# Kernel optimization log

Measured on AMD Instinct MI355X. Metric: run time of the kernel, lower is better.

The kernel has to match this reference:

```python
import jax, jax.numpy as jnp
import numpy as np

N_CODES = 1024
CODE_DIM = 256
B, T = 64, 1024


def setup_inputs() -> dict:
    key = jax.random.key(0)
    k1, k2 = jax.random.split(key)
    inputs = jax.random.normal(k1, (B, CODE_DIM, T), dtype=jnp.float32)
    embed = jax.random.normal(k2, (N_CODES, CODE_DIM), dtype=jnp.float32)
    return {"inputs": inputs, "embed": embed, "training": 0}


def reference(inputs, embed, training):
    # inputs: [B, D, T] -> [B, T, D]
    x = jnp.transpose(inputs, (0, 2, 1))
    Bsz, Tlen, D = x.shape
    flat = x.reshape(-1, D)  # [N, D], N = B*T
    distances = (
        jnp.sum(flat * flat, axis=1, keepdims=True)
        - 2.0 * jnp.matmul(flat, embed.T)
        + jnp.sum(embed * embed, axis=1)
    )  # [N, n_codes]
    encoding_indices = jnp.argmin(distances, axis=1)  # [N]
    # gather instead of one-hot matmul (same math)
    quantized = embed[encoding_indices].reshape(x.shape)  # [B, T, D]

    sg = jax.lax.stop_gradient
    codebook_loss = jnp.mean((sg(quantized) - x) ** 2)
    cmt_loss = jnp.mean((quantized - sg(x)) ** 2)
    loss = codebook_loss + cmt_loss * 0.2

    # straight-through estimator
    quantized_st = x + sg(quantized - x)
    quantized_out = jnp.transpose(quantized_st, (0, 2, 1))  # [B, D, T]

    # avg one-hot probabilities via bincount-style scatter-add
    n = flat.shape[0]
    counts = jnp.zeros((N_CODES,), dtype=flat.dtype).at[encoding_indices].add(1.0)
    avg_probs = counts / n
    perplexity = jnp.exp(-jnp.sum(avg_probs * jnp.log(avg_probs + 1e-10)))

    encoding_indices_out = encoding_indices.reshape(Bsz, -1, 1)
    return (quantized_out, loss, cmt_loss, encoding_indices_out, perplexity)
```

## Files before the change

kernel.cpp:

```cpp
#include <hip/hip_runtime.h>

#define B_ 64
#define D_ 256
#define T_ 1024
#define NC_ 1024
#define DT_ (D_ * T_)
#define NPTS_ (B_ * T_)

#define QSZ_   16777216
#define LOSS_OFF 16777216
#define CMT_OFF  16777217
#define IDX_OFF  16777218
#define PERP_OFF 16842754

typedef _Float16 half8 __attribute__((ext_vector_type(8)));
typedef float f32x4 __attribute__((ext_vector_type(4)));

__global__ void prep_embed(const float* __restrict__ embed,
                           _Float16* __restrict__ ehi,
                           _Float16* __restrict__ elo,
                           float* __restrict__ normf) {
  int g = blockIdx.x;
  int tid = threadIdx.x;
  int w = tid >> 6, l = tid & 63;

#pragma unroll
  for (int ii = 0; ii < 2; ++ii) {
    int kc = w * 2 + ii;
    int code = g * 16 + (l & 15);
    int k0 = kc * 32 + (l >> 4) * 8;
    const float* src = embed + (size_t)code * D_ + k0;
    half8 hh, ll;
#pragma unroll
    for (int j = 0; j < 8; ++j) {
      float v = src[j];
      _Float16 h = (_Float16)v;
      _Float16 lo = (_Float16)(v - (float)h);
      hh[j] = h;
      ll[j] = lo;
    }
    size_t off = ((size_t)(g * 8 + kc) * 64 + l) * 8;
    *(half8*)(ehi + off) = hh;
    *(half8*)(elo + off) = ll;
  }

  int code = g * 16 + (tid >> 4);
  int ks = (tid & 15) * 16;
  const float* src = embed + (size_t)code * D_ + ks;
  double s = 0.0;
#pragma unroll
  for (int j = 0; j < 16; ++j) {
    double v = src[j];
    s += v * v;
  }
#pragma unroll
  for (int m = 1; m < 16; m <<= 1) s += __shfl_xor(s, m, 64);
  if ((tid & 15) == 0) normf[code] = (float)s;
}

__device__ __forceinline__ void gld_lds16(const _Float16* gsrc_lane,
                                          _Float16* lds_base) {
  __builtin_amdgcn_global_load_lds(
      (const __attribute__((address_space(1))) void*)gsrc_lane,
      (__attribute__((address_space(3))) void*)lds_base, 16, 0, 0);
}

__global__ __launch_bounds__(256, 3) void argmin_kernel(
    const float* __restrict__ inputs, const _Float16* __restrict__ ehi,
    const _Float16* __restrict__ elo, const float* __restrict__ normf,
    float* __restrict__ idx_out, int* __restrict__ counts,
    double* __restrict__ mse_acc) {
  __shared__ _Float16 ldsB[2][8192];
  __shared__ float normf_lds[1024];
  __shared__ double xn2w[64];

  int tid = threadIdx.x;
  int blk = blockIdx.x;
  int b = blk >> 4, t0 = (blk & 15) * 64;
  int w = tid >> 6, l = tid & 63;

  half8 ah[8], al[8];
  double xn2p = 0.0;
  {
    const float* xsrc = inputs + (size_t)b * DT_ + t0 + w * 16 + (l & 15);
    int kbase = (l >> 4) * 8;
#pragma unroll
    for (int kc = 0; kc < 8; ++kc) {
      half8 hh, ll;
#pragma unroll
      for (int j = 0; j < 8; ++j) {
        float v = xsrc[(size_t)(kc * 32 + kbase + j) * T_];
        xn2p += (double)v * v;
        _Float16 h = (_Float16)v;
        _Float16 lo = (_Float16)(v - (float)h);
        hh[j] = h;
        ll[j] = lo;
      }
      ah[kc] = hh;
      al[kc] = ll;
    }
  }
  xn2p += __shfl_xor(xn2p, 16, 64);
  xn2p += __shfl_xor(xn2p, 32, 64);
  if (l < 16) xn2w[w * 16 + l] = xn2p;

  ((float4*)normf_lds)[tid] = ((const float4*)normf)[tid];
#pragma unroll
  for (int i = 0; i < 2; ++i) {
    int kc = w * 2 + i;
    size_t off = ((size_t)kc * 64 + l) * 8;
    gld_lds16(ehi + off, &ldsB[0][kc * 512]);
    gld_lds16(elo + off, &ldsB[0][4096 + kc * 512]);
  }
  __syncthreads();

  float bestv[4];
  int besti[4];
#pragma unroll
  for (int j = 0; j < 4; ++j) {
    bestv[j] = 1e30f;
    besti[j] = 0;
  }

#pragma unroll 1
  for (int t = 0; t < 64; ++t) {
    int cur = t & 1, nxt = cur ^ 1;
    if (t < 63) {
#pragma unroll
      for (int i = 0; i < 2; ++i) {
        int kc = w * 2 + i;
        size_t off = ((size_t)((t + 1) * 8 + kc) * 64 + l) * 8;
        gld_lds16(ehi + off, &ldsB[nxt][kc * 512]);
        gld_lds16(elo + off, &ldsB[nxt][4096 + kc * 512]);
      }
    }

    f32x4 acc = (f32x4){0.f, 0.f, 0.f, 0.f};
#pragma unroll
    for (int kc = 0; kc < 8; ++kc) {
      half8 bh = *(const half8*)&ldsB[cur][(kc * 64 + l) * 8];
      half8 bl = *(const half8*)&ldsB[cur][4096 + (kc * 64 + l) * 8];
      acc = __builtin_amdgcn_mfma_f32_16x16x32_f16(ah[kc], bh, acc, 0, 0, 0);
      acc = __builtin_amdgcn_mfma_f32_16x16x32_f16(al[kc], bh, acc, 0, 0, 0);
      acc = __builtin_amdgcn_mfma_f32_16x16x32_f16(ah[kc], bl, acc, 0, 0, 0);
    }

    {
      int c = t * 16 + (l & 15);
      float nf = normf_lds[c];
#pragma unroll
      for (int j = 0; j < 4; ++j) {
        float df = fmaf(-2.0f, acc[j], nf);
        if (df < bestv[j]) {
          bestv[j] = df;
          besti[j] = c;
        }
      }
    }
    __syncthreads();
  }

#pragma unroll
  for (int msk = 1; msk < 16; msk <<= 1) {
#pragma unroll
    for (int j = 0; j < 4; ++j) {
      float ov = __shfl_xor(bestv[j], msk, 64);
      int oi = __shfl_xor(besti[j], msk, 64);
      if (ov < bestv[j] || (ov == bestv[j] && oi < besti[j])) {
        bestv[j] = ov;
        besti[j] = oi;
      }
    }
  }

  if ((l & 15) == 0) {
    float4 iw;
    double s = 0.0;
#pragma unroll
    for (int j = 0; j < 4; ++j) {
      int p = (l >> 4) * 4 + j;
      iw[j == 0 ? 0 : (j == 1 ? 1 : (j == 2 ? 2 : 3))] = (float)besti[j];
      atomicAdd(&counts[besti[j]], 1);
      s += xn2w[w * 16 + p] + (double)bestv[j];
    }
    *(float4*)&idx_out[blk * 64 + w * 16 + (l >> 4) * 4] = iw;
    s += __shfl_xor(s, 16, 64);
    s += __shfl_xor(s, 32, 64);
    if (l == 0) atomicAdd(mse_acc, s);
  }
}

__global__ __launch_bounds__(256) void quantize_kernel(
    const float* __restrict__ embed, const float* __restrict__ idx_f,
    float* __restrict__ qout) {
  __shared__ float qs[64 * 257];
  __shared__ int lidx[64];

  int tid = threadIdx.x;
  int bx = blockIdx.x;
  int b = bx >> 4;
  int t0 = (bx & 15) * 64;

  if (tid < 64) lidx[tid] = (int)idx_f[b * T_ + t0 + tid];
  __syncthreads();

#pragma unroll 4
  for (int p = 0; p < 64; ++p) {
    qs[p * 257 + tid] = embed[(size_t)lidx[p] * D_ + tid];
  }
  __syncthreads();

  size_t base = (size_t)b * DT_ + t0;
#pragma unroll 4
  for (int i = 0; i < 64; ++i) {
    int d = i * 4 + (tid >> 6);
    int p = tid & 63;
    qout[base + (size_t)d * T_ + p] = qs[p * 257 + d];
  }
}

__global__ void finalize_kernel(const int* __restrict__ counts,
                                const double* __restrict__ mse_acc,
                                float* __restrict__ out) {
  int tid = threadIdx.x;
  double p = (double)counts[tid] / (double)NPTS_;
  double s = p * log(p + 1e-10);
  for (int m = 32; m; m >>= 1) s += __shfl_down(s, m, 64);
  __shared__ double red[16];
  if ((tid & 63) == 0) red[tid >> 6] = s;
  __syncthreads();
  if (tid == 0) {
    double tot = 0.0;
    for (int i = 0; i < 16; ++i) tot += red[i];
    double mse = *mse_acc / (double)QSZ_;
    out[LOSS_OFF] = (float)(mse * 1.2);
    out[CMT_OFF] = (float)mse;
    out[PERP_OFF] = (float)exp(-tot);
  }
}

extern "C" void kernel_launch(void* const* d_in, const int* in_sizes, int n_in,
                              void* d_out, int out_size, void* d_ws,
                              size_t ws_size, hipStream_t stream) {
  const float* inputs = (const float*)d_in[0];
  const float* embed = (const float*)d_in[1];
  float* out = (float*)d_out;

  char* ws = (char*)d_ws;
  _Float16* ehi = (_Float16*)ws;
  _Float16* elo = (_Float16*)(ws + 524288);
  float* normf = (float*)(ws + 1048576);
  int* counts = (int*)(ws + 1048576 + 4096);
  double* mse = (double*)(ws + 1048576 + 8192);

  hipMemsetAsync(ws + 1048576 + 4096, 0, 4096 + 8, stream);

  prep_embed<<<64, 256, 0, stream>>>(embed, ehi, elo, normf);
  argmin_kernel<<<1024, 256, 0, stream>>>(inputs, ehi, elo, normf,
                                          out + IDX_OFF, counts, mse);
  quantize_kernel<<<1024, 256, 0, stream>>>(embed, out + IDX_OFF, out);
  finalize_kernel<<<1, 1024, 0, stream>>>(counts, mse, out);
}
```

Before: 176.8 us.

## Process two 16-row M tiles per wave in argmin to reuse codebook fragments

Each wave now holds A fragments for 32 points instead of 16 and runs two accumulator chains over every codebook tile loaded into LDS. The number of blocks is halved. This amortizes LDS reads of the codebook and the per-block codebook streaming over twice as many points, and interleaves independent MFMAs to hide their latency. In exchange it doubles A-fragment registers and lowers the occupancy target from 3 to 2 blocks per CU. With 512 blocks the grid may also underfill the GPU.

```diff
diff --git a/kernel.cpp b/kernel.cpp
--- a/kernel.cpp
+++ b/kernel.cpp
@@ -65,44 +65,52 @@
       (__attribute__((address_space(3))) void*)lds_base, 16, 0, 0);
 }
 
-__global__ __launch_bounds__(256, 3) void argmin_kernel(
+__global__ __launch_bounds__(256, 2) void argmin_kernel(
     const float* __restrict__ inputs, const _Float16* __restrict__ ehi,
     const _Float16* __restrict__ elo, const float* __restrict__ normf,
     float* __restrict__ idx_out, int* __restrict__ counts,
     double* __restrict__ mse_acc) {
   __shared__ _Float16 ldsB[2][8192];
   __shared__ float normf_lds[1024];
-  __shared__ double xn2w[64];
+  __shared__ double xn2w[128];
 
   int tid = threadIdx.x;
   int blk = blockIdx.x;
-  int b = blk >> 4, t0 = (blk & 15) * 64;
+  int b = blk >> 3, t0 = (blk & 7) * 128;
   int w = tid >> 6, l = tid & 63;
 
-  half8 ah[8], al[8];
-  double xn2p = 0.0;
+  half8 ah[2][8], al[2][8];
+  double xn2p0 = 0.0, xn2p1 = 0.0;
   {
-    const float* xsrc = inputs + (size_t)b * DT_ + t0 + w * 16 + (l & 15);
-    int kbase = (l >> 4) * 8;
-#pragma unroll
-    for (int kc = 0; kc < 8; ++kc) {
-      half8 hh, ll;
-#pragma unroll
-      for (int j = 0; j < 8; ++j) {
-        float v = xsrc[(size_t)(kc * 32 + kbase + j) * T_];
-        xn2p += (double)v * v;
-        _Float16 h = (_Float16)v;
-        _Float16 lo = (_Float16)(v - (float)h);
-        hh[j] = h;
-        ll[j] = lo;
-      }
-      ah[kc] = hh;
-      al[kc] = ll;
-    }
-  }
-  xn2p += __shfl_xor(xn2p, 16, 64);
-  xn2p += __shfl_xor(xn2p, 32, 64);
-  if (l < 16) xn2w[w * 16 + l] = xn2p;
+    int kq = (l >> 4) * 8;
+    const float* xcol = inputs + (size_t)b * DT_ + t0 + w * 32 + (l & 15);
+#pragma unroll
+    for (int m = 0; m < 2; ++m) {
+      const float* src = xcol + m * 16;
+#pragma unroll
+      for (int kc = 0; kc < 8; ++kc) {
+        half8 hh, ll;
+#pragma unroll
+        for (int j = 0; j < 8; ++j) {
+          float v = src[(size_t)(kc * 32 + kq + j) * T_];
+          if (m == 0) xn2p0 += (double)v * v; else xn2p1 += (double)v * v;
+          _Float16 h = (_Float16)v;
+          hh[j] = h;
+          ll[j] = (_Float16)(v - (float)h);
+        }
+        ah[m][kc] = hh;
+        al[m][kc] = ll;
+      }
+    }
+  }
+  xn2p0 += __shfl_xor(xn2p0, 16, 64);
+  xn2p0 += __shfl_xor(xn2p0, 32, 64);
+  xn2p1 += __shfl_xor(xn2p1, 16, 64);
+  xn2p1 += __shfl_xor(xn2p1, 32, 64);
+  if (l < 16) {
+    xn2w[w * 32 + l] = xn2p0;
+    xn2w[w * 32 + 16 + l] = xn2p1;
+  }
 
   ((float4*)normf_lds)[tid] = ((const float4*)normf)[tid];
 #pragma unroll
@@ -114,13 +122,15 @@
   }
   __syncthreads();
 
-  float bestv[4];
-  int besti[4];
-#pragma unroll
-  for (int j = 0; j < 4; ++j) {
-    bestv[j] = 1e30f;
-    besti[j] = 0;
-  }
+  float bestv[2][4];
+  int besti[2][4];
+#pragma unroll
+  for (int m = 0; m < 2; ++m)
+#pragma unroll
+    for (int j = 0; j < 4; ++j) {
+      bestv[m][j] = 1e30f;
+      besti[m][j] = 0;
+    }
 
 #pragma unroll 1
   for (int t = 0; t < 64; ++t) {
@@ -135,14 +145,18 @@
       }
     }
 
-    f32x4 acc = (f32x4){0.f, 0.f, 0.f, 0.f};
+    f32x4 acc0 = (f32x4){0.f, 0.f, 0.f, 0.f};
+    f32x4 acc1 = (f32x4){0.f, 0.f, 0.f, 0.f};
 #pragma unroll
     for (int kc = 0; kc < 8; ++kc) {
       half8 bh = *(const half8*)&ldsB[cur][(kc * 64 + l) * 8];
       half8 bl = *(const half8*)&ldsB[cur][4096 + (kc * 64 + l) * 8];
-      acc = __builtin_amdgcn_mfma_f32_16x16x32_f16(ah[kc], bh, acc, 0, 0, 0);
-      acc = __builtin_amdgcn_mfma_f32_16x16x32_f16(al[kc], bh, acc, 0, 0, 0);
-      acc = __builtin_amdgcn_mfma_f32_16x16x32_f16(ah[kc], bl, acc, 0, 0, 0);
+      acc0 = __builtin_amdgcn_mfma_f32_16x16x32_f16(ah[0][kc], bh, acc0, 0, 0, 0);
+      acc1 = __builtin_amdgcn_mfma_f32_16x16x32_f16(ah[1][kc], bh, acc1, 0, 0, 0);
+      acc0 = __builtin_amdgcn_mfma_f32_16x16x32_f16(al[0][kc], bh, acc0, 0, 0, 0);
+      acc1 = __builtin_amdgcn_mfma_f32_16x16x32_f16(al[1][kc], bh, acc1, 0, 0, 0);
+      acc0 = __builtin_amdgcn_mfma_f32_16x16x32_f16(ah[0][kc], bl, acc0, 0, 0, 0);
+      acc1 = __builtin_amdgcn_mfma_f32_16x16x32_f16(ah[1][kc], bl, acc1, 0, 0, 0);
     }
 
     {
@@ -150,10 +164,15 @@
       float nf = normf_lds[c];
 #pragma unroll
       for (int j = 0; j < 4; ++j) {
-        float df = fmaf(-2.0f, acc[j], nf);
-        if (df < bestv[j]) {
-          bestv[j] = df;
-          besti[j] = c;
+        float df0 = fmaf(-2.0f, acc0[j], nf);
+        if (df0 < bestv[0][j]) {
+          bestv[0][j] = df0;
+          besti[0][j] = c;
+        }
+        float df1 = fmaf(-2.0f, acc1[j], nf);
+        if (df1 < bestv[1][j]) {
+          bestv[1][j] = df1;
+          besti[1][j] = c;
         }
       }
     }
@@ -163,27 +182,33 @@
 #pragma unroll
   for (int msk = 1; msk < 16; msk <<= 1) {
 #pragma unroll
-    for (int j = 0; j < 4; ++j) {
-      float ov = __shfl_xor(bestv[j], msk, 64);
-      int oi = __shfl_xor(besti[j], msk, 64);
-      if (ov < bestv[j] || (ov == bestv[j] && oi < besti[j])) {
-        bestv[j] = ov;
-        besti[j] = oi;
-      }
-    }
+    for (int m = 0; m < 2; ++m)
+#pragma unroll
+      for (int j = 0; j < 4; ++j) {
+        float ov = __shfl_xor(bestv[m][j], msk, 64);
+        int oi = __shfl_xor(besti[m][j], msk, 64);
+        if (ov < bestv[m][j] || (ov == bestv[m][j] && oi < besti[m][j])) {
+          bestv[m][j] = ov;
+          besti[m][j] = oi;
+        }
+      }
   }
 
   if ((l & 15) == 0) {
-    float4 iw;
+    int q = l >> 4;
     double s = 0.0;
 #pragma unroll
-    for (int j = 0; j < 4; ++j) {
-      int p = (l >> 4) * 4 + j;
-      iw[j == 0 ? 0 : (j == 1 ? 1 : (j == 2 ? 2 : 3))] = (float)besti[j];
-      atomicAdd(&counts[besti[j]], 1);
-      s += xn2w[w * 16 + p] + (double)bestv[j];
-    }
-    *(float4*)&idx_out[blk * 64 + w * 16 + (l >> 4) * 4] = iw;
+    for (int m = 0; m < 2; ++m) {
+      float4 iw;
+#pragma unroll
+      for (int j = 0; j < 4; ++j) {
+        int bi = besti[m][j];
+        iw[j] = (float)bi;
+        atomicAdd(&counts[bi], 1);
+        s += xn2w[w * 32 + m * 16 + q * 4 + j] + (double)bestv[m][j];
+      }
+      *(float4*)&idx_out[blk * 128 + w * 32 + m * 16 + q * 4] = iw;
+    }
     s += __shfl_xor(s, 16, 64);
     s += __shfl_xor(s, 32, 64);
     if (l == 0) atomicAdd(mse_acc, s);
@@ -256,8 +281,8 @@
   hipMemsetAsync(ws + 1048576 + 4096, 0, 4096 + 8, stream);
 
   prep_embed<<<64, 256, 0, stream>>>(embed, ehi, elo, normf);
-  argmin_kernel<<<1024, 256, 0, stream>>>(inputs, ehi, elo, normf,
-                                          out + IDX_OFF, counts, mse);
+  argmin_kernel<<<512, 256, 0, stream>>>(inputs, ehi, elo, normf,
+                                         out + IDX_OFF, counts, mse);
   quantize_kernel<<<1024, 256, 0, stream>>>(embed, out + IDX_OFF, out);
   finalize_kernel<<<1, 1024, 0, stream>>>(counts, mse, out);
 }
```

Result: faster. 167.5 us (-5.2%).
